# Performance work log

Hardware: AMD Instinct MI355X
Metric: run time of the kernel (lower is better)

The kernel has to match this reference:

```python
import jax, jax.numpy as jnp
import numpy as np

N, T, U, D, V = 8, 200, 100, 512, 500


def setup_inputs() -> dict:
    key = jax.random.key(0)
    k1, k2, k3, k4 = jax.random.split(key, 4)
    encoder_out = jax.random.normal(k1, (N, T, D), dtype=jnp.float32)
    decoder_out = jax.random.normal(k2, (N, U, D), dtype=jnp.float32)
    # nn.Linear(input_dim, output_dim): weight (V, D), bias (V,)
    bound = 1.0 / np.sqrt(D)
    W = jax.random.uniform(k3, (V, D), minval=-bound, maxval=bound, dtype=jnp.float32)
    b = jax.random.uniform(k4, (V,), minval=-bound, maxval=bound, dtype=jnp.float32)
    return {"encoder_out": encoder_out, "decoder_out": decoder_out, "W": W, "b": b}


def reference(encoder_out, decoder_out, W, b):
    # broadcast add: (N,T,1,D) + (N,1,U,D) -> (N,T,U,D)
    x = encoder_out[:, :, None, :] + decoder_out[:, None, :, :]
    activations = jnp.tanh(x)
    # linear: (N,T,U,D) @ (D,V) + b -> (N,T,U,V)
    logits = jnp.einsum("ntud,vd->ntuv", activations, W) + b
    return logits
```

## Files before the change

### kernel.cpp

```cpp
#include <hip/hip_runtime.h>
#include <hip/hip_bf16.h>


#define NB 8
#define TT 200
#define UU 100
#define DD 512
#define VV 500
#define VP 512
#define BM 64
#define BK 32
#define KSTEPS 16
#define THREADS 256
#define LDA 40
#define MROWS (NB*TT*UU)
#define MBLOCKS (MROWS/BM)

typedef __attribute__((ext_vector_type(4))) float         f32x4;
typedef __attribute__((ext_vector_type(8))) short         s16x8;
typedef __attribute__((ext_vector_type(4))) unsigned int  u32x4;

#define RAW_BAR() do { asm volatile("s_waitcnt lgkmcnt(0)" ::: "memory"); \
                       __builtin_amdgcn_s_barrier(); } while (0)

__device__ __forceinline__ unsigned short f2bf(float f) {
    unsigned int u = __builtin_bit_cast(unsigned int, f);
    u = (u + 0x7FFFu + ((u >> 16) & 1u)) >> 16;
    return (unsigned short)u;
}

__device__ __forceinline__ unsigned int cvt_pk_bf16(float a, float b) {
    unsigned int r;
    asm("v_cvt_pk_bf16_f32 %0, %1, %2" : "=v"(r) : "v"(a), "v"(b));
    return r;
}

__device__ __forceinline__ float fast_tanh(float x) {
    float e = __builtin_amdgcn_exp2f(x * 2.88539008177793f);
    return __builtin_fmaf(-2.0f, __builtin_amdgcn_rcpf(e + 1.0f), 1.0f);
}

__global__ void prep_w(const float* __restrict__ W, unsigned short* __restrict__ Wt) {
    int idx = blockIdx.x * 256 + threadIdx.x;
    int k = idx & 511;
    int v = idx >> 9;
    float val = (v < VV) ? W[v * DD + k] : 0.0f;
    Wt[(k >> 5) * (VP * BK) + v * BK + (k & 31)] = f2bf(val);
}

#define KBODY(kc, CUR, NXT, BC, BNX)                                          \
  {                                                                           \
       \
    if ((kc) < KSTEPS - 1) {                                                  \
      _Pragma("unroll")                                                       \
      for (int f = 0; f < 8; ++f)                                             \
        BNX[f] = *(const s16x8*)(wptr + ((kc)+1) * (VP * BK) + f * (16*BK));  \
    }                                                                         \
               \
    f32x4 ne0, ne1, nd0, nd1;                                                 \
    if ((kc) < KSTEPS - 2) {                                                  \
      const float* e2 = ep + ((kc)+2) * BK;                                   \
      const float* d2 = dp + ((kc)+2) * BK;                                   \
      ne0 = *(const f32x4*)(e2);  ne1 = *(const f32x4*)(e2 + 4);              \
      nd0 = *(const f32x4*)(d2);  nd1 = *(const f32x4*)(d2 + 4);              \
    }                                                                         \
                                               \
    s16x8 aF[4];                                                              \
    _Pragma("unroll")                                                         \
    for (int m = 0; m < 4; ++m)                                               \
      aF[m] = *(const s16x8*)(&CUR[(m * 16 + lr) * LDA + lk * 8]);            \
                                             \
    if ((kc) < KSTEPS - 1) {                                                  \
      u32x4 wds;                                                              \
      wds[0] = cvt_pk_bf16(fast_tanh(e0[0]+d0[0]), fast_tanh(e0[1]+d0[1]));   \
      wds[1] = cvt_pk_bf16(fast_tanh(e0[2]+d0[2]), fast_tanh(e0[3]+d0[3]));   \
      wds[2] = cvt_pk_bf16(fast_tanh(e1[0]+d1[0]), fast_tanh(e1[1]+d1[1]));   \
      wds[3] = cvt_pk_bf16(fast_tanh(e1[2]+d1[2]), fast_tanh(e1[3]+d1[3]));   \
      *(u32x4*)(&NXT[srow * LDA + sk]) = wds;                                 \
    }                                                                         \
                                                         \
    if ((kc) < KSTEPS - 2) {                                                  \
      e0 = ne0; e1 = ne1; d0 = nd0; d1 = nd1;                                 \
    }                                                                         \
                        \
    __builtin_amdgcn_s_setprio(1);                                            \
    _Pragma("unroll")                                                         \
    for (int m = 0; m < 4; ++m)                                               \
      _Pragma("unroll")                                                       \
      for (int f = 0; f < 8; ++f)                                             \
        acc[m][f] = __builtin_amdgcn_mfma_f32_16x16x32_bf16(aF[m], BC[f],     \
                                                            acc[m][f],0,0,0); \
    __builtin_amdgcn_s_setprio(0);                                            \
                \
    if ((kc) < KSTEPS - 1) RAW_BAR();                                         \
  }

__global__ __launch_bounds__(THREADS, 2) void joiner_kernel(
    const float* __restrict__ enc, const float* __restrict__ dec,
    const unsigned short* __restrict__ Wt, const float* __restrict__ bias,
    float* __restrict__ out)
{
    __shared__ __align__(16) char smem[32000];
    unsigned short* lA0 = (unsigned short*)smem;
    unsigned short* lA1 = (unsigned short*)(smem + BM * LDA * 2);

    const int tid  = threadIdx.x;
    const int mb   = blockIdx.x;
    const int lane = tid & 63;
    const int wn   = tid >> 6;
    const int lr   = lane & 15;
    const int lk   = lane >> 4;

    const int srow = tid >> 2;
    const int sk   = (tid & 3) << 3;

    int r   = mb * BM + srow;
    int n   = r / (TT * UU);
    int rem = r - n * (TT * UU);
    int t   = rem / UU;
    int u   = rem - t * UU;
    const float* ep = enc + (n * TT + t) * DD + sk;
    const float* dp = dec + (n * UU + u) * DD + sk;

    const unsigned short* wptr = Wt + (wn * 128 + lr) * BK + lk * 8;

    f32x4 e0, e1, d0, d1;
    s16x8 b0[8], b1[8];

    e0 = *(const f32x4*)(ep);     e1 = *(const f32x4*)(ep + 4);
    d0 = *(const f32x4*)(dp);     d1 = *(const f32x4*)(dp + 4);
    #pragma unroll
    for (int f = 0; f < 8; ++f)
        b0[f] = *(const s16x8*)(wptr + f * (16 * BK));
    {
        u32x4 wds;
        wds[0] = cvt_pk_bf16(fast_tanh(e0[0]+d0[0]), fast_tanh(e0[1]+d0[1]));
        wds[1] = cvt_pk_bf16(fast_tanh(e0[2]+d0[2]), fast_tanh(e0[3]+d0[3]));
        wds[2] = cvt_pk_bf16(fast_tanh(e1[0]+d1[0]), fast_tanh(e1[1]+d1[1]));
        wds[3] = cvt_pk_bf16(fast_tanh(e1[2]+d1[2]), fast_tanh(e1[3]+d1[3]));
        *(u32x4*)(&lA0[srow * LDA + sk]) = wds;
    }
    e0 = *(const f32x4*)(ep + BK);     e1 = *(const f32x4*)(ep + BK + 4);
    d0 = *(const f32x4*)(dp + BK);     d1 = *(const f32x4*)(dp + BK + 4);
    RAW_BAR();

    f32x4 acc[4][8];
    #pragma unroll
    for (int m = 0; m < 4; ++m)
        #pragma unroll
        for (int f = 0; f < 8; ++f)
            acc[m][f] = (f32x4){0.f, 0.f, 0.f, 0.f};

    #pragma unroll
    for (int kk = 0; kk < KSTEPS; kk += 2) {
        KBODY(kk,     lA0, lA1, b0, b1)
        KBODY(kk + 1, lA1, lA0, b1, b0)
    }

    float bv[8];
    #pragma unroll
    for (int f = 0; f < 8; ++f) {
        int v = wn * 128 + f * 16 + lr;
        bv[f] = (v < VV) ? bias[v] : 0.0f;
    }

    float* lchunk = (float*)smem;
    float* outbase = out + (long)mb * BM * VV;

    for (int m = 0; m < 4; ++m) {
        RAW_BAR();
        #pragma unroll
        for (int f = 0; f < 8; ++f) {
            int v = wn * 128 + f * 16 + lr;
            if (v < VV) {
                #pragma unroll
                for (int q = 0; q < 4; ++q)
                    lchunk[(lk * 4 + q) * VV + v] = acc[m][f][q] + bv[f];
            }
        }
        RAW_BAR();
        float* dst = outbase + m * 16 * VV;
        #pragma unroll
        for (int i = 0; i < 8; ++i) {
            int c = i * THREADS + tid;
            if (c < 2000)
                *(f32x4*)(dst + c * 4) = *(const f32x4*)(lchunk + c * 4);
        }
    }
}

extern "C" void kernel_launch(void* const* d_in, const int* in_sizes, int n_in,
                              void* d_out, int out_size, void* d_ws, size_t ws_size,
                              hipStream_t stream) {
    const float* enc = (const float*)d_in[0];
    const float* dec = (const float*)d_in[1];
    const float* W   = (const float*)d_in[2];
    const float* b   = (const float*)d_in[3];
    float* out = (float*)d_out;
    unsigned short* Wt = (unsigned short*)d_ws;

    prep_w<<<dim3((VP * DD) / 256), dim3(256), 0, stream>>>(W, Wt);
    joiner_kernel<<<dim3(MBLOCKS), dim3(THREADS), 0, stream>>>(enc, dec, Wt, b, out);
}
```

Baseline: 131.4 us.

## Interleave MFMA groups with loads and tanh staging in the K loop

Splits each K step's 32 MFMAs into four row-groups and spreads the W-fragment global loads, enc/dec prefetches, LDS A-fragment reads and tanh/bf16 conversion between them. The first A fragment of the next step is read right after the barrier. The aim is to hide load latency and VALU transcendental work behind matrix-core execution instead of issuing all of it before a single MFMA burst. It also spreads register lifetimes differently, which may raise or lower pressure under the 2-waves occupancy bound.

```diff
diff --git a/kernel.cpp b/kernel.cpp
--- a/kernel.cpp
+++ b/kernel.cpp
@@ -50,49 +50,77 @@
 
 #define KBODY(kc, CUR, NXT, BC, BNX)                                          \
   {                                                                           \
-       \
-    if ((kc) < KSTEPS - 1) {                                                  \
-      _Pragma("unroll")                                                       \
-      for (int f = 0; f < 8; ++f)                                             \
-        BNX[f] = *(const s16x8*)(wptr + ((kc)+1) * (VP * BK) + f * (16*BK));  \
-    }                                                                         \
-               \
+    s16x8 aF1, aF2, aF3;                                                      \
+    u32x4 wds;                                                                \
     f32x4 ne0, ne1, nd0, nd1;                                                 \
+                                   \
+    if ((kc) < KSTEPS - 1) {                                                  \
+      BNX[0] = *(const s16x8*)(wptr + ((kc)+1) * (VP * BK) + 0 * (16*BK));    \
+      BNX[1] = *(const s16x8*)(wptr + ((kc)+1) * (VP * BK) + 1 * (16*BK));    \
+    }                                                                         \
     if ((kc) < KSTEPS - 2) {                                                  \
       const float* e2 = ep + ((kc)+2) * BK;                                   \
+      ne0 = *(const f32x4*)(e2);  ne1 = *(const f32x4*)(e2 + 4);              \
+    }                                                                         \
+    aF1 = *(const s16x8*)(&CUR[(1 * 16 + lr) * LDA + lk * 8]);                \
+    wds[0] = cvt_pk_bf16(fast_tanh(e0[0]+d0[0]), fast_tanh(e0[1]+d0[1]));     \
+    wds[1] = cvt_pk_bf16(fast_tanh(e0[2]+d0[2]), fast_tanh(e0[3]+d0[3]));     \
+    __builtin_amdgcn_s_setprio(1);                                            \
+    _Pragma("unroll")                                                         \
+    for (int f = 0; f < 8; ++f)                                               \
+      acc[0][f] = __builtin_amdgcn_mfma_f32_16x16x32_bf16(a0, BC[f],          \
+                                                          acc[0][f],0,0,0);   \
+    __builtin_amdgcn_s_setprio(0);                                            \
+                                  \
+    if ((kc) < KSTEPS - 1) {                                                  \
+      BNX[2] = *(const s16x8*)(wptr + ((kc)+1) * (VP * BK) + 2 * (16*BK));    \
+      BNX[3] = *(const s16x8*)(wptr + ((kc)+1) * (VP * BK) + 3 * (16*BK));    \
+    }                                                                         \
+    if ((kc) < KSTEPS - 2) {                                                  \
       const float* d2 = dp + ((kc)+2) * BK;                                   \
-      ne0 = *(const f32x4*)(e2);  ne1 = *(const f32x4*)(e2 + 4);              \
       nd0 = *(const f32x4*)(d2);  nd1 = *(const f32x4*)(d2 + 4);              \
     }                                                                         \
-                                               \
-    s16x8 aF[4];                                                              \
-    _Pragma("unroll")                                                         \
-    for (int m = 0; m < 4; ++m)                                               \
-      aF[m] = *(const s16x8*)(&CUR[(m * 16 + lr) * LDA + lk * 8]);            \
-                                             \
-    if ((kc) < KSTEPS - 1) {                                                  \
-      u32x4 wds;                                                              \
-      wds[0] = cvt_pk_bf16(fast_tanh(e0[0]+d0[0]), fast_tanh(e0[1]+d0[1]));   \
-      wds[1] = cvt_pk_bf16(fast_tanh(e0[2]+d0[2]), fast_tanh(e0[3]+d0[3]));   \
-      wds[2] = cvt_pk_bf16(fast_tanh(e1[0]+d1[0]), fast_tanh(e1[1]+d1[1]));   \
-      wds[3] = cvt_pk_bf16(fast_tanh(e1[2]+d1[2]), fast_tanh(e1[3]+d1[3]));   \
+    aF2 = *(const s16x8*)(&CUR[(2 * 16 + lr) * LDA + lk * 8]);                \
+    wds[2] = cvt_pk_bf16(fast_tanh(e1[0]+d1[0]), fast_tanh(e1[1]+d1[1]));     \
+    wds[3] = cvt_pk_bf16(fast_tanh(e1[2]+d1[2]), fast_tanh(e1[3]+d1[3]));     \
+    __builtin_amdgcn_s_setprio(1);                                            \
+    _Pragma("unroll")                                                         \
+    for (int f = 0; f < 8; ++f)                                               \
+      acc[1][f] = __builtin_amdgcn_mfma_f32_16x16x32_bf16(aF1, BC[f],         \
+                                                          acc[1][f],0,0,0);   \
+    __builtin_amdgcn_s_setprio(0);                                            \
+                                  \
+    if ((kc) < KSTEPS - 1) {                                                  \
+      BNX[4] = *(const s16x8*)(wptr + ((kc)+1) * (VP * BK) + 4 * (16*BK));    \
+      BNX[5] = *(const s16x8*)(wptr + ((kc)+1) * (VP * BK) + 5 * (16*BK));    \
       *(u32x4*)(&NXT[srow * LDA + sk]) = wds;                                 \
     }                                                                         \
-                                                         \
+    aF3 = *(const s16x8*)(&CUR[(3 * 16 + lr) * LDA + lk * 8]);                \
+    __builtin_amdgcn_s_setprio(1);                                            \
+    _Pragma("unroll")                                                         \
+    for (int f = 0; f < 8; ++f)                                               \
+      acc[2][f] = __builtin_amdgcn_mfma_f32_16x16x32_bf16(aF2, BC[f],         \
+                                                          acc[2][f],0,0,0);   \
+    __builtin_amdgcn_s_setprio(0);                                            \
+                                  \
+    if ((kc) < KSTEPS - 1) {                                                  \
+      BNX[6] = *(const s16x8*)(wptr + ((kc)+1) * (VP * BK) + 6 * (16*BK));    \
+      BNX[7] = *(const s16x8*)(wptr + ((kc)+1) * (VP * BK) + 7 * (16*BK));    \
+    }                                                                         \
     if ((kc) < KSTEPS - 2) {                                                  \
       e0 = ne0; e1 = ne1; d0 = nd0; d1 = nd1;                                 \
     }                                                                         \
-                        \
-    __builtin_amdgcn_s_setprio(1);                                            \
-    _Pragma("unroll")                                                         \
-    for (int m = 0; m < 4; ++m)                                               \
-      _Pragma("unroll")                                                       \
-      for (int f = 0; f < 8; ++f)                                             \
-        acc[m][f] = __builtin_amdgcn_mfma_f32_16x16x32_bf16(aF[m], BC[f],     \
-                                                            acc[m][f],0,0,0); \
-    __builtin_amdgcn_s_setprio(0);                                            \
-                \
-    if ((kc) < KSTEPS - 1) RAW_BAR();                                         \
+    __builtin_amdgcn_s_setprio(1);                                            \
+    _Pragma("unroll")                                                         \
+    for (int f = 0; f < 8; ++f)                                               \
+      acc[3][f] = __builtin_amdgcn_mfma_f32_16x16x32_bf16(aF3, BC[f],         \
+                                                          acc[3][f],0,0,0);   \
+    __builtin_amdgcn_s_setprio(0);                                            \
+                  \
+    if ((kc) < KSTEPS - 1) {                                                  \
+      RAW_BAR();                                                              \
+      a0 = *(const s16x8*)(&NXT[(0 * 16 + lr) * LDA + lk * 8]);               \
+    }                                                                         \
   }
 
 __global__ __launch_bounds__(THREADS, 2) void joiner_kernel(
@@ -126,6 +154,7 @@
 
     f32x4 e0, e1, d0, d1;
     s16x8 b0[8], b1[8];
+    s16x8 a0;
 
     e0 = *(const f32x4*)(ep);     e1 = *(const f32x4*)(ep + 4);
     d0 = *(const f32x4*)(dp);     d1 = *(const f32x4*)(dp + 4);
@@ -143,6 +172,7 @@
     e0 = *(const f32x4*)(ep + BK);     e1 = *(const f32x4*)(ep + BK + 4);
     d0 = *(const f32x4*)(dp + BK);     d1 = *(const f32x4*)(dp + BK + 4);
     RAW_BAR();
+    a0 = *(const s16x8*)(&lA0[(0 * 16 + lr) * LDA + lk * 8]);
 
     f32x4 acc[4][8];
     #pragma unroll
```

Result: no change. 131.6 us (+0.2%).
